# Optimization experiments

Hardware: AMD Instinct MI355X
Metric: run time of the kernel (lower is better)

## Reference

```python
import jax, jax.numpy as jnp
import numpy as np

N = 50000        # nodes
E = 800000       # edges
F_IN = 32        # float features (x also carries 1 trailing cell-id column)
CELL_DIM = 16
NUM_CELLS = 854
C = 64           # out_channels
H0, H1 = 2, 1    # heads schedule for num_layers=2 -> [2, 1]
D_IN = F_IN + CELL_DIM  # 48, GAT input dim after cell embedding concat
NEG_SLOPE = 0.2  # PyG GATConv default negative_slope


def setup_inputs() -> dict:
    key = jax.random.key(0)
    ks = jax.random.split(key, 14)
    base = jax.random.normal(ks[0], (N, F_IN), jnp.float32)
    cell_ids = jax.random.randint(ks[1], (N,), 0, NUM_CELLS)
    x = jnp.concatenate([base, cell_ids.astype(jnp.float32)[:, None]], axis=1)
    edge_index = jax.random.randint(ks[2], (2, E), 0, N, dtype=jnp.int32)
    s = lambda f: 1.0 / np.sqrt(f)
    emb = jax.random.normal(ks[3], (NUM_CELLS, CELL_DIM), jnp.float32)
    W0 = jax.random.normal(ks[4], (D_IN, H0 * C), jnp.float32) * s(D_IN)
    a_src0 = jax.random.normal(ks[5], (H0, C), jnp.float32) * s(C)
    a_dst0 = jax.random.normal(ks[6], (H0, C), jnp.float32) * s(C)
    b0 = jnp.zeros((C,), jnp.float32)
    ln_g = jnp.ones((C,), jnp.float32)
    ln_b = jnp.zeros((C,), jnp.float32)
    W1 = jax.random.normal(ks[7], (C, H1 * C), jnp.float32) * s(C)
    a_src1 = jax.random.normal(ks[8], (H1, C), jnp.float32) * s(C)
    a_dst1 = jax.random.normal(ks[9], (H1, C), jnp.float32) * s(C)
    b1 = jnp.zeros((C,), jnp.float32)
    return {"x": x, "edge_index": edge_index, "emb": emb,
            "W0": W0, "a_src0": a_src0, "a_dst0": a_dst0, "b0": b0,
            "ln_g": ln_g, "ln_b": ln_b,
            "W1": W1, "a_src1": a_src1, "a_dst1": a_dst1, "b1": b1}


def gat_layer(h_in, src, dst, W, a_src, a_dst, b, heads):
    # h_in: [N, D]; src/dst: [E'] (self-loops already appended)
    h = (h_in @ W).reshape(N, heads, C)                 # [N, H, C]
    alpha_s = jnp.einsum('nhc,hc->nh', h, a_src)        # [N, H]
    alpha_d = jnp.einsum('nhc,hc->nh', h, a_dst)
    e = jax.nn.leaky_relu(alpha_s[src] + alpha_d[dst], NEG_SLOPE)  # [E', H]
    # segment softmax over incoming edges of each dst node
    m = jax.ops.segment_max(e, dst, num_segments=N)     # [N, H]
    ex = jnp.exp(e - m[dst])
    denom = jax.ops.segment_sum(ex, dst, num_segments=N)
    alpha = ex / denom[dst]                             # [E', H]
    msg = h[src] * alpha[:, :, None]                    # [E', H, C]
    out = jax.ops.segment_sum(msg, dst, num_segments=N) # [N, H, C]
    return out.mean(axis=1) + b                         # concat=False -> mean over heads


def layer_norm(x, g, b):
    mu = x.mean(-1, keepdims=True)
    var = ((x - mu) ** 2).mean(-1, keepdims=True)
    return (x - mu) * jax.lax.rsqrt(var + 1e-5) * g + b


def reference(x, edge_index, emb, W0, a_src0, a_dst0, b0, ln_g, ln_b,
              W1, a_src1, a_dst1, b1):
    base = x[:, :-1]
    cell_ids = x[:, -1].astype(jnp.int32)
    h = jnp.concatenate([base, emb[cell_ids]], axis=1)  # [N, 48]
    # add self-loops (PyG GATConv default add_self_loops=True)
    loop = jnp.arange(N, dtype=edge_index.dtype)
    src = jnp.concatenate([edge_index[0], loop])
    dst = jnp.concatenate([edge_index[1], loop])
    h = gat_layer(h, src, dst, W0, a_src0, a_dst0, b0, H0)
    h = jax.nn.elu(layer_norm(h, ln_g, ln_b))           # dropout is identity at eval
    h = gat_layer(h, src, dst, W1, a_src1, a_dst1, b1, H1)
    return h
```

## Files before the change

### kernel.cpp

```cpp
#include <hip/hip_runtime.h>
#include <hip/hip_bf16.h>

#define N_NODES 50000
#define N_EDGES 800000
#define F_IN 32
#define CELL_DIM 16
#define D_IN 48
#define X_STRIDE 33
#define NUM_CELLS 854
#define NEG_SLOPE 0.2f
#define NODE0_BLOCKS 2048
#define MERGE_BLOCKS 1563
#define EDGE_BLOCKS 3125
#define NXCD 8
#define BWX 16
#define BW 48
#define W 24
#define NP 12

typedef unsigned int uint;
typedef unsigned short ushort;

static __device__ __forceinline__ uint f2b(float f) {
  uint x = __float_as_uint(f);
  return (x + 0x7fffu + ((x >> 16) & 1u)) >> 16;
}
static __device__ __forceinline__ float b2f_lo(uint w) { return __uint_as_float(w << 16); }
static __device__ __forceinline__ float b2f_hi(uint w) { return __uint_as_float(w & 0xffff0000u); }
static __device__ __forceinline__ float lrelu(float e) { return fmaxf(e, NEG_SLOPE * e); }


__global__ __launch_bounds__(256) void k_bfill(const int* __restrict__ ei,
                                               int* __restrict__ cnt,
                                               ushort* __restrict__ bkt) {
  int e = blockIdx.x * 256 + threadIdx.x;
  if (e >= N_EDGES) return;
  uint xcc;
  asm volatile("s_getreg_b32 %0, hwreg(HW_REG_XCC_ID)" : "=s"(xcc));
  xcc &= (NXCD - 1);
  int s = ei[e], d = ei[N_EDGES + e];
  int p = atomicAdd(&cnt[xcc * N_NODES + d], 1);
  if (p < BWX) bkt[(xcc * N_NODES + d) * BWX + p] = (ushort)s;
}


__global__ __launch_bounds__(256) void k_node0(const float* __restrict__ x,
                                               const float* __restrict__ emb,
                                               const float* __restrict__ W0,
                                               const float* __restrict__ asrc,
                                               const float* __restrict__ adst,
                                               ushort* __restrict__ h0u,
                                               float* __restrict__ as0, float* __restrict__ ad0) {
  int tid = threadIdx.x;
  __shared__ float hin[8][48];
  int lane = tid & 63, wid = tid >> 6;
  int h = wid & 1;
  int q = wid >> 1;
  float w0r[D_IN];
#pragma unroll
  for (int k = 0; k < D_IN; ++k) w0r[k] = W0[k * 128 + h * 64 + lane];
  float av_s = asrc[h * 64 + lane], av_d = adst[h * 64 + lane];

  for (int g = blockIdx.x; g < N_NODES / 8; g += NODE0_BLOCKS) {
    int nb = g * 8;
#pragma unroll
    for (int j = 0; j < 2; ++j) {
      int loc = 2 * wid + j;
      int n = nb + loc;
      float t = 0.f;
      if (lane < 33) t = x[n * X_STRIDE + lane];
      int cid = (int)__shfl(t, 32, 64);
      cid = cid < 0 ? 0 : (cid >= NUM_CELLS ? NUM_CELLS - 1 : cid);
      if (lane >= 32 && lane < 48) t = emb[cid * CELL_DIM + (lane - 32)];
      if (lane < 48) hin[loc][lane] = t;
    }
    __syncthreads();
#pragma unroll
    for (int j = 0; j < 4; ++j) {
      int loc = 4 * q + j;
      int n = nb + loc;
      const float4* hp = (const float4*)hin[loc];
      float acc = 0.f;
#pragma unroll
      for (int k4 = 0; k4 < 12; ++k4) {
        float4 hh = hp[k4];
        acc = fmaf(hh.x, w0r[4 * k4 + 0], acc);
        acc = fmaf(hh.y, w0r[4 * k4 + 1], acc);
        acc = fmaf(hh.z, w0r[4 * k4 + 2], acc);
        acc = fmaf(hh.w, w0r[4 * k4 + 3], acc);
      }
      h0u[(n * 64 + lane) * 2 + h] = (ushort)f2b(acc);
      float sa = acc * av_s, sd = acc * av_d;
#pragma unroll
      for (int o = 32; o >= 1; o >>= 1) {
        sa += __shfl_xor(sa, o, 64);
        sd += __shfl_xor(sd, o, 64);
      }
      if (lane == 0) {
        as0[n * 2 + h] = sa;
        ad0[n * 2 + h] = sd;
      }
    }
    __syncthreads();
  }
}


__global__ __launch_bounds__(256) void k_merge(const int* __restrict__ cnt,
                                               const ushort* __restrict__ bkt,
                                               const float2* __restrict__ as0v,
                                               const float2* __restrict__ ad0v,
                                               int* __restrict__ cntc,
                                               uint2* __restrict__ bktw) {
  int tid = threadIdx.x;
  int n = blockIdx.x * 32 + (tid >> 3);
  if (n >= N_NODES) return;
  int xg = tid & 7;
  int cx = min(cnt[xg * N_NODES + n], BWX);
  int sc = cx;
#pragma unroll
  for (int o = 1; o < 8; o <<= 1) {
    int t = __shfl_up(sc, o, 64);
    if ((tid & 7) >= o) sc += t;
  }
  int total = __shfl(sc, (tid & 63) | 7, 64);
  int base = sc - cx;
  float2 ad = ad0v[n];
  const ushort* src = bkt + (xg * N_NODES + n) * BWX;
  for (int k = 0; k < cx; ++k) {
    uint s = src[k];
    float2 a = as0v[s];
    uint wp = f2b(__expf(lrelu(a.x + ad.x))) | (f2b(__expf(lrelu(a.y + ad.y))) << 16);
    int slot = base + k;
    if (slot < BW) bktw[n * BW + slot] = make_uint2(s, wp);
  }
  if (xg == 7) cntc[n] = min(total, BW);
}


__global__ __launch_bounds__(256) void k_agg0(const int* __restrict__ cntc,
                                              const uint2* __restrict__ bktw,
                                              const float2* __restrict__ as0v,
                                              const float2* __restrict__ ad0v,
                                              const uint* __restrict__ h0p,
                                              const float* __restrict__ b0,
                                              const float* __restrict__ lng,
                                              const float* __restrict__ lnb,
                                              const float* __restrict__ W1,
                                              const float* __restrict__ asrc1,
                                              const float* __restrict__ adst1,
                                              ushort* __restrict__ h1b,
                                              float* __restrict__ as1, float* __restrict__ ad1) {
  __shared__ uint gbuf[4][W * 64];
  __shared__ float yb[4][64];
  int tid = threadIdx.x;
  int lane = tid & 63, wl = tid >> 6;
  int n = blockIdx.x * 4 + wl;
  int nE = cntc[n];
  int items = nE + 1;
  float2 a_n = as0v[n];
  float2 ad = ad0v[n];
  uint selfw = f2b(__expf(lrelu(a_n.x + ad.x))) | (f2b(__expf(lrelu(a_n.y + ad.y))) << 16);
  float acc0 = 0.f, acc1 = 0.f, den0 = 0.f, den1 = 0.f;
  uint* gb = gbuf[wl];

  for (int w0 = 0; w0 < items; w0 += W) {
    int idx = w0 + lane;
    uint2 rec = make_uint2(0u, 0u);
    if (lane < W && idx < items)
      rec = (idx < nE) ? bktw[n * BW + idx] : make_uint2((uint)n, selfw);
#pragma unroll
    for (int j = 0; j < W; ++j) {
      uint sx = (uint)__builtin_amdgcn_readlane((int)rec.x, j);
      __builtin_amdgcn_global_load_lds((const uint*)(h0p + sx * 64u + (uint)lane),
                                       gb + j * 64, 4, 0, 0);
    }
    asm volatile("s_waitcnt vmcnt(0)" ::: "memory");
    __builtin_amdgcn_sched_barrier(0);
#pragma unroll
    for (int j = 0; j < W; ++j) {
      uint wy = (uint)__builtin_amdgcn_readlane((int)rec.y, j);
      uint h = gb[j * 64 + lane];
      float w;
      w = b2f_lo(wy); acc0 += w * b2f_lo(h); den0 += w;
      w = b2f_hi(wy); acc1 += w * b2f_hi(h); den1 += w;
    }
    asm volatile("s_waitcnt lgkmcnt(0)" ::: "memory");
    __builtin_amdgcn_sched_barrier(0);
  }

  float v = 0.5f * (acc0 / den0 + acc1 / den1) + b0[lane];
  float mu = v;
#pragma unroll
  for (int o = 32; o >= 1; o >>= 1) mu += __shfl_xor(mu, o, 64);
  mu *= (1.0f / 64.0f);
  float d = v - mu;
  float vr = d * d;
#pragma unroll
  for (int o = 32; o >= 1; o >>= 1) vr += __shfl_xor(vr, o, 64);
  vr *= (1.0f / 64.0f);
  float y = d * rsqrtf(vr + 1e-5f) * lng[lane] + lnb[lane];
  y = y > 0.f ? y : expm1f(y);
  yb[wl][lane] = y;
  const float4* yp = (const float4*)yb[wl];
  float q0 = 0.f, q1 = 0.f, q2 = 0.f, q3 = 0.f;
#pragma unroll
  for (int k4 = 0; k4 < 16; ++k4) {
    float4 yy = yp[k4];
    q0 = fmaf(yy.x, W1[(4 * k4 + 0) * 64 + lane], q0);
    q1 = fmaf(yy.y, W1[(4 * k4 + 1) * 64 + lane], q1);
    q2 = fmaf(yy.z, W1[(4 * k4 + 2) * 64 + lane], q2);
    q3 = fmaf(yy.w, W1[(4 * k4 + 3) * 64 + lane], q3);
  }
  float h1v = (q0 + q1) + (q2 + q3);
  h1b[n * 64 + lane] = (ushort)f2b(h1v);
  float sa = h1v * asrc1[lane];
  float sdv = h1v * adst1[lane];
#pragma unroll
  for (int o = 32; o >= 1; o >>= 1) {
    sa += __shfl_xor(sa, o, 64);
    sdv += __shfl_xor(sdv, o, 64);
  }
  if (lane == 0) {
    as1[n] = sa;
    ad1[n] = sdv;
  }
}


__global__ __launch_bounds__(256) void k_agg1(const int* __restrict__ cntc,
                                              const uint2* __restrict__ bktw,
                                              const ushort* __restrict__ h1b,
                                              const float* __restrict__ as1,
                                              const float* __restrict__ ad1,
                                              const float* __restrict__ b1,
                                              float* __restrict__ out) {
  __shared__ uint gbuf[4][NP * 64];
  int tid = threadIdx.x;
  int lane = tid & 63, wl = tid >> 6;
  int n = blockIdx.x * 4 + wl;
  int nE = cntc[n];
  int items = nE + 1;
  float adv = ad1[n];
  float acc = 0.f, den = 0.f;
  uint* gb = gbuf[wl];
  const ushort* gbs = (const ushort*)gb;
  uint hl = lane & 31;
  int half = lane >> 5;

  for (int w0 = 0; w0 < items; w0 += W) {
    int idx = w0 + lane;
    uint s = 0u;
    float wv = 0.f;
    if (lane < W && idx < items) {
      s = (idx < nE) ? bktw[n * BW + idx].x : (uint)n;
      wv = __expf(lrelu(as1[s] + adv));
    }
#pragma unroll
    for (int j = 0; j < NP; ++j) {
      uint sxA = (uint)__builtin_amdgcn_readlane((int)s, 2 * j);
      uint sxB = (uint)__builtin_amdgcn_readlane((int)s, 2 * j + 1);
      uint sx2 = half ? sxB : sxA;
      __builtin_amdgcn_global_load_lds((const uint*)(h1b + sx2 * 64u) + hl,
                                       gb + j * 64, 4, 0, 0);
    }
    asm volatile("s_waitcnt vmcnt(0)" ::: "memory");
    __builtin_amdgcn_sched_barrier(0);
#pragma unroll
    for (int j = 0; j < NP; ++j) {
      float wA = __uint_as_float(
          (uint)__builtin_amdgcn_readlane((int)__float_as_uint(wv), 2 * j));
      float wB = __uint_as_float(
          (uint)__builtin_amdgcn_readlane((int)__float_as_uint(wv), 2 * j + 1));
      uint hA = (uint)gbs[j * 128 + lane];
      uint hB = (uint)gbs[j * 128 + 64 + lane];
      acc = fmaf(wA, __uint_as_float(hA << 16), acc);
      den += wA;
      acc = fmaf(wB, __uint_as_float(hB << 16), acc);
      den += wB;
    }
    asm volatile("s_waitcnt lgkmcnt(0)" ::: "memory");
    __builtin_amdgcn_sched_barrier(0);
  }
  out[n * 64 + lane] = acc / den + b1[lane];
}


extern "C" void kernel_launch(void* const* d_in, const int* in_sizes, int n_in,
                              void* d_out, int out_size, void* d_ws, size_t ws_size,
                              hipStream_t stream) {
  const float* x    = (const float*)d_in[0];
  const int*   ei   = (const int*)d_in[1];
  const float* emb  = (const float*)d_in[2];
  const float* W0   = (const float*)d_in[3];
  const float* as0w = (const float*)d_in[4];
  const float* ad0w = (const float*)d_in[5];
  const float* b0   = (const float*)d_in[6];
  const float* lng  = (const float*)d_in[7];
  const float* lnb  = (const float*)d_in[8];
  const float* W1   = (const float*)d_in[9];
  const float* as1w = (const float*)d_in[10];
  const float* ad1w = (const float*)d_in[11];
  const float* b1   = (const float*)d_in[12];
  float* out = (float*)d_out;

  ushort* bkt  = (ushort*)d_ws;
  ushort* h1b  = (ushort*)d_ws;
  int*    cnt  = (int*)((char*)d_ws + (size_t)NXCD * N_NODES * BWX * 2);
  float*  as1  = (float*)cnt;
  float*  ad1  = as1 + N_NODES;
  uint2*  bktw = (uint2*)((char*)cnt + (size_t)NXCD * N_NODES * 4);
  int*    cntc = (int*)(bktw + (size_t)N_NODES * BW);
  float*  as0  = (float*)(cntc + N_NODES);
  float*  ad0  = as0 + N_NODES * 2;
  uint*   h0p  = (uint*)(ad0 + N_NODES * 2);

  hipMemsetAsync(cnt, 0, NXCD * N_NODES * sizeof(int), stream);
  k_bfill<<<EDGE_BLOCKS, 256, 0, stream>>>(ei, cnt, bkt);
  k_node0<<<NODE0_BLOCKS, 256, 0, stream>>>(x, emb, W0, as0w, ad0w, (ushort*)h0p, as0, ad0);
  k_merge<<<MERGE_BLOCKS, 256, 0, stream>>>(cnt, bkt, (const float2*)as0, (const float2*)ad0,
                                            cntc, bktw);
  k_agg0<<<N_NODES / 4, 256, 0, stream>>>(cntc, bktw, (const float2*)as0, (const float2*)ad0,
                                          h0p, b0, lng, lnb, W1, as1w, ad1w, h1b, as1, ad1);
  k_agg1<<<N_NODES / 4, 256, 0, stream>>>(cntc, bktw, h1b, as1, ad1, b1, out);
}
```

Before: 252.8 us.

## Replace fixed-width padded edge buckets with compacted CSR via prefix scan

Adds a two-kernel prefix scan over the per-node bucket counts (self-loop included) and builds compacted CSR arrays: 16-bit source ids and packed bf16 weights in separate arrays. The merge kernel now writes the self-loop entry directly, and both aggregation kernels read contiguous per-node ranges instead of padded 48-wide uint2 slots. This cuts the footprint and scattered accesses of the edge list, at the cost of two extra small kernel launches. Per-XCD truncation at 16 entries is kept, while the old 48-total cap is removed.

```diff
diff --git a/kernel.cpp b/kernel.cpp
--- a/kernel.cpp
+++ b/kernel.cpp
@@ -3,18 +3,19 @@
 
 #define N_NODES 50000
 #define N_EDGES 800000
+#define E_TOT 850000
 #define F_IN 32
 #define CELL_DIM 16
 #define D_IN 48
 #define X_STRIDE 33
 #define NUM_CELLS 854
 #define NEG_SLOPE 0.2f
+#define SCAN_BLOCKS 49
 #define NODE0_BLOCKS 2048
 #define MERGE_BLOCKS 1563
 #define EDGE_BLOCKS 3125
 #define NXCD 8
 #define BWX 16
-#define BW 48
 #define W 24
 #define NP 12
 
@@ -44,6 +45,65 @@
 }
 
 
+__global__ __launch_bounds__(1024) void k_scan1(const int* __restrict__ cnt,
+                                                int* __restrict__ off,
+                                                int* __restrict__ bsum) {
+  __shared__ int ws[16];
+  int tid = threadIdx.x;
+  int lane = tid & 63, wid = tid >> 6;
+  int i = blockIdx.x * 1024 + tid;
+  int v = 0;
+  if (i < N_NODES) {
+    v = 1;
+#pragma unroll
+    for (int x = 0; x < NXCD; ++x) v += min(cnt[x * N_NODES + i], BWX);
+  }
+  int sc = v;
+#pragma unroll
+  for (int o = 1; o < 64; o <<= 1) {
+    int t = __shfl_up(sc, o, 64);
+    if (lane >= o) sc += t;
+  }
+  if (lane == 63) ws[wid] = sc;
+  __syncthreads();
+  if (tid < 16) {
+    int w = ws[tid];
+    int s = w;
+#pragma unroll
+    for (int o = 1; o < 16; o <<= 1) {
+      int t = __shfl_up(s, o, 64);
+      if (tid >= o) s += t;
+    }
+    ws[tid] = s - w;
+  }
+  __syncthreads();
+  int excl = sc - v + ws[wid];
+  if (i < N_NODES) off[i] = excl;
+  if (tid == 1023) bsum[blockIdx.x] = excl + v;
+}
+
+__global__ __launch_bounds__(1024) void k_scan23(int* __restrict__ off,
+                                                 const int* __restrict__ bsum) {
+  __shared__ int carry_s;
+  int tid = threadIdx.x;
+  if (tid < 64) {
+    int v = (tid < SCAN_BLOCKS) ? bsum[tid] : 0;
+    int s = v;
+#pragma unroll
+    for (int o = 1; o < 64; o <<= 1) {
+      int t = __shfl_up(s, o, 64);
+      if (tid >= o) s += t;
+    }
+    if (tid == (int)blockIdx.x) carry_s = s - v;
+    if (blockIdx.x == 0 && tid == SCAN_BLOCKS - 1) off[N_NODES] = s;
+  }
+  __syncthreads();
+  int carry = carry_s;
+  int i = blockIdx.x * 1024 + tid;
+  if (i < N_NODES) off[i] += carry;
+}
+
+
 __global__ __launch_bounds__(256) void k_node0(const float* __restrict__ x,
                                                const float* __restrict__ emb,
                                                const float* __restrict__ W0,
@@ -108,10 +168,11 @@
 
 __global__ __launch_bounds__(256) void k_merge(const int* __restrict__ cnt,
                                                const ushort* __restrict__ bkt,
+                                               const int* __restrict__ off,
                                                const float2* __restrict__ as0v,
                                                const float2* __restrict__ ad0v,
-                                               int* __restrict__ cntc,
-                                               uint2* __restrict__ bktw) {
+                                               ushort* __restrict__ srcs,
+                                               uint* __restrict__ wts) {
   int tid = threadIdx.x;
   int n = blockIdx.x * 32 + (tid >> 3);
   if (n >= N_NODES) return;
@@ -124,24 +185,29 @@
     if ((tid & 7) >= o) sc += t;
   }
   int total = __shfl(sc, (tid & 63) | 7, 64);
-  int base = sc - cx;
+  int base = off[n] + (sc - cx);
   float2 ad = ad0v[n];
   const ushort* src = bkt + (xg * N_NODES + n) * BWX;
   for (int k = 0; k < cx; ++k) {
     uint s = src[k];
     float2 a = as0v[s];
     uint wp = f2b(__expf(lrelu(a.x + ad.x))) | (f2b(__expf(lrelu(a.y + ad.y))) << 16);
-    int slot = base + k;
-    if (slot < BW) bktw[n * BW + slot] = make_uint2(s, wp);
-  }
-  if (xg == 7) cntc[n] = min(total, BW);
-}
-
-
-__global__ __launch_bounds__(256) void k_agg0(const int* __restrict__ cntc,
-                                              const uint2* __restrict__ bktw,
-                                              const float2* __restrict__ as0v,
-                                              const float2* __restrict__ ad0v,
+    srcs[base + k] = (ushort)s;
+    wts[base + k] = wp;
+  }
+  if (xg == 7) {
+    float2 a = as0v[n];
+    uint wp = f2b(__expf(lrelu(a.x + ad.x))) | (f2b(__expf(lrelu(a.y + ad.y))) << 16);
+    int slot = off[n] + total;
+    srcs[slot] = (ushort)n;
+    wts[slot] = wp;
+  }
+}
+
+
+__global__ __launch_bounds__(256) void k_agg0(const int* __restrict__ off,
+                                              const ushort* __restrict__ srcs,
+                                              const uint* __restrict__ wts,
                                               const uint* __restrict__ h0p,
                                               const float* __restrict__ b0,
                                               const float* __restrict__ lng,
@@ -156,22 +222,20 @@
   int tid = threadIdx.x;
   int lane = tid & 63, wl = tid >> 6;
   int n = blockIdx.x * 4 + wl;
-  int nE = cntc[n];
-  int items = nE + 1;
-  float2 a_n = as0v[n];
-  float2 ad = ad0v[n];
-  uint selfw = f2b(__expf(lrelu(a_n.x + ad.x))) | (f2b(__expf(lrelu(a_n.y + ad.y))) << 16);
+  int i0 = off[n], i1 = off[n + 1];
   float acc0 = 0.f, acc1 = 0.f, den0 = 0.f, den1 = 0.f;
   uint* gb = gbuf[wl];
 
-  for (int w0 = 0; w0 < items; w0 += W) {
+  for (int w0 = i0; w0 < i1; w0 += W) {
     int idx = w0 + lane;
-    uint2 rec = make_uint2(0u, 0u);
-    if (lane < W && idx < items)
-      rec = (idx < nE) ? bktw[n * BW + idx] : make_uint2((uint)n, selfw);
+    uint s = 0u, wy = 0u;
+    if (lane < W && idx < i1) {
+      s = (uint)srcs[idx];
+      wy = wts[idx];
+    }
 #pragma unroll
     for (int j = 0; j < W; ++j) {
-      uint sx = (uint)__builtin_amdgcn_readlane((int)rec.x, j);
+      uint sx = (uint)__builtin_amdgcn_readlane((int)s, j);
       __builtin_amdgcn_global_load_lds((const uint*)(h0p + sx * 64u + (uint)lane),
                                        gb + j * 64, 4, 0, 0);
     }
@@ -179,11 +243,11 @@
     __builtin_amdgcn_sched_barrier(0);
 #pragma unroll
     for (int j = 0; j < W; ++j) {
-      uint wy = (uint)__builtin_amdgcn_readlane((int)rec.y, j);
+      uint wyj = (uint)__builtin_amdgcn_readlane((int)wy, j);
       uint h = gb[j * 64 + lane];
       float w;
-      w = b2f_lo(wy); acc0 += w * b2f_lo(h); den0 += w;
-      w = b2f_hi(wy); acc1 += w * b2f_hi(h); den1 += w;
+      w = b2f_lo(wyj); acc0 += w * b2f_lo(h); den0 += w;
+      w = b2f_hi(wyj); acc1 += w * b2f_hi(h); den1 += w;
     }
     asm volatile("s_waitcnt lgkmcnt(0)" ::: "memory");
     __builtin_amdgcn_sched_barrier(0);
@@ -228,8 +292,8 @@
 }
 
 
-__global__ __launch_bounds__(256) void k_agg1(const int* __restrict__ cntc,
-                                              const uint2* __restrict__ bktw,
+__global__ __launch_bounds__(256) void k_agg1(const int* __restrict__ off,
+                                              const ushort* __restrict__ srcs,
                                               const ushort* __restrict__ h1b,
                                               const float* __restrict__ as1,
                                               const float* __restrict__ ad1,
@@ -239,8 +303,7 @@
   int tid = threadIdx.x;
   int lane = tid & 63, wl = tid >> 6;
   int n = blockIdx.x * 4 + wl;
-  int nE = cntc[n];
-  int items = nE + 1;
+  int i0 = off[n], i1 = off[n + 1];
   float adv = ad1[n];
   float acc = 0.f, den = 0.f;
   uint* gb = gbuf[wl];
@@ -248,12 +311,12 @@
   uint hl = lane & 31;
   int half = lane >> 5;
 
-  for (int w0 = 0; w0 < items; w0 += W) {
+  for (int w0 = i0; w0 < i1; w0 += W) {
     int idx = w0 + lane;
     uint s = 0u;
     float wv = 0.f;
-    if (lane < W && idx < items) {
-      s = (idx < nE) ? bktw[n * BW + idx].x : (uint)n;
+    if (lane < W && idx < i1) {
+      s = (uint)srcs[idx];
       wv = __expf(lrelu(as1[s] + adv));
     }
 #pragma unroll
@@ -309,18 +372,22 @@
   int*    cnt  = (int*)((char*)d_ws + (size_t)NXCD * N_NODES * BWX * 2);
   float*  as1  = (float*)cnt;
   float*  ad1  = as1 + N_NODES;
-  uint2*  bktw = (uint2*)((char*)cnt + (size_t)NXCD * N_NODES * 4);
-  int*    cntc = (int*)(bktw + (size_t)N_NODES * BW);
-  float*  as0  = (float*)(cntc + N_NODES);
+  int*    off  = (int*)((char*)cnt + (size_t)NXCD * N_NODES * 4);
+  int*    bsum = off + N_NODES + 1;
+  ushort* srcs = (ushort*)(bsum + 64);
+  uint*   wts  = (uint*)(srcs + E_TOT);
+  float*  as0  = (float*)(wts + E_TOT);
   float*  ad0  = as0 + N_NODES * 2;
   uint*   h0p  = (uint*)(ad0 + N_NODES * 2);
 
   hipMemsetAsync(cnt, 0, NXCD * N_NODES * sizeof(int), stream);
   k_bfill<<<EDGE_BLOCKS, 256, 0, stream>>>(ei, cnt, bkt);
+  k_scan1<<<SCAN_BLOCKS, 1024, 0, stream>>>(cnt, off, bsum);
+  k_scan23<<<SCAN_BLOCKS, 1024, 0, stream>>>(off, bsum);
   k_node0<<<NODE0_BLOCKS, 256, 0, stream>>>(x, emb, W0, as0w, ad0w, (ushort*)h0p, as0, ad0);
-  k_merge<<<MERGE_BLOCKS, 256, 0, stream>>>(cnt, bkt, (const float2*)as0, (const float2*)ad0,
-                                            cntc, bktw);
-  k_agg0<<<N_NODES / 4, 256, 0, stream>>>(cntc, bktw, (const float2*)as0, (const float2*)ad0,
-                                          h0p, b0, lng, lnb, W1, as1w, ad1w, h1b, as1, ad1);
-  k_agg1<<<N_NODES / 4, 256, 0, stream>>>(cntc, bktw, h1b, as1, ad1, b1, out);
-}
+  k_merge<<<MERGE_BLOCKS, 256, 0, stream>>>(cnt, bkt, off, (const float2*)as0,
+                                            (const float2*)ad0, srcs, wts);
+  k_agg0<<<N_NODES / 4, 256, 0, stream>>>(off, srcs, wts, h0p, b0, lng, lnb, W1,
+                                          as1w, ad1w, h1b, as1, ad1);
+  k_agg1<<<N_NODES / 4, 256, 0, stream>>>(off, srcs, h1b, as1, ad1, b1, out);
+}
```

After: 250.0 us. No clear change (-1.1%).
